# Optimization experiments

Hardware: AMD Instinct MI355X
Metric: run time of the kernel (lower is better)

## Reference

```python
import jax, jax.numpy as jnp
import numpy as np

N, C, H, W = 10, 512, 40, 40
HW = H * W
OUT_CH = 128
EPS = 1e-12

def _l2norm(x, axis):
    # matches F.normalize: v / max(||v||_2, eps)
    n = jnp.sqrt(jnp.sum(x * x, axis=axis, keepdims=True))
    return x / jnp.maximum(n, EPS)

def _conv(x, w, b, pad):
    y = jax.lax.conv_general_dilated(
        x, w, window_strides=(1, 1), padding=[(pad, pad), (pad, pad)],
        dimension_numbers=('NCHW', 'OIHW', 'NCHW'))
    return y + b[None, :, None, None]

def setup_inputs() -> dict:
    key = jax.random.key(0)
    ks = jax.random.split(key, 6)
    feats = jax.random.normal(ks[0], (N, C, H, W), jnp.float32)
    SISMs = jax.random.uniform(ks[1], (N, 1, H, W), jnp.float32)
    # ResNetBlock(HW -> 128) params (Kaiming-uniform-ish fan-in bounds)
    s1 = float(1.0 / np.sqrt(HW * 9))
    s2 = float(1.0 / np.sqrt(OUT_CH * 9))
    ss = float(1.0 / np.sqrt(HW))
    w1 = jax.random.uniform(ks[2], (OUT_CH, HW, 3, 3), jnp.float32, -s1, s1)
    b1 = jnp.zeros((OUT_CH,), jnp.float32)
    w2 = jax.random.uniform(ks[3], (OUT_CH, OUT_CH, 3, 3), jnp.float32, -s2, s2)
    b2 = jnp.zeros((OUT_CH,), jnp.float32)
    ws = jax.random.uniform(ks[4], (OUT_CH, HW, 1, 1), jnp.float32, -ss, ss)
    bs = jnp.zeros((OUT_CH,), jnp.float32)
    return dict(feats=feats, SISMs=SISMs, w1=w1, b1=b1, w2=w2, b2=b2, ws=ws, bs=bs)

def reference(feats, SISMs, w1, b1, w2, b2, ws, bs):
    # SISMs supplied at (H,W): bilinear resize w/ align_corners=True at same size is identity
    NFs = _l2norm(feats, axis=1)                                   # (N,C,H,W)
    SIVs = _l2norm(jnp.mean(NFs * SISMs, axis=(-1, -2)), axis=1)   # (N,C)
    # CFM: 1x1 conv of NFs with SIVs as filters -> (N,N,H,W)
    cm = jnp.einsum('nchw,mc->nmhw', NFs, SIVs).reshape(N, N, HW)
    cm = _l2norm(cm, axis=2)
    corr = jnp.einsum('nmk,npk->nmp', cm, cm)                      # (N,N,N)
    wv = jax.nn.softmax(jnp.sum(corr, axis=2), axis=1)             # (N,N)
    CSA = jnp.sum(cm * wv[:, :, None], axis=1)                     # (N,HW)
    mn = jnp.min(CSA, axis=1, keepdims=True)
    mx = jnp.max(CSA, axis=1, keepdims=True)
    CSA = (CSA - mn) / (mx - mn + EPS)
    CSA_maps = CSA.reshape(N, 1, H, W)
    # self-correlation features: (N, HW, H, W)
    NFf = NFs.reshape(N, C, HW)
    SCFs = jnp.einsum('nci,ncj->nij', NFf, NFf).reshape(N, HW, H, W)
    # reorder channels by descending CSA evidence
    idx = jnp.argsort(-CSA, axis=1)                                # (N,HW)
    RSCFs = jnp.take_along_axis(SCFs, idx[:, :, None, None], axis=1)
    x = RSCFs * CSA_maps
    # ResNetBlock: relu(conv2(relu(conv1(x))) + shortcut_1x1(x))
    h = jax.nn.relu(_conv(x, w1, b1, 1))
    h = _conv(h, w2, b2, 1)
    sc = _conv(x, ws, bs, 0)
    return jax.nn.relu(h + sc)
```

## Files before the change

### kernel.cpp

```cpp
#include <hip/hip_runtime.h>
#include <hip/hip_bf16.h>
#include <math.h>

typedef short short8 __attribute__((ext_vector_type(8)));
typedef short short4v __attribute__((ext_vector_type(4)));
typedef float f32x4 __attribute__((ext_vector_type(4)));
typedef __hip_bfloat16 bf16;

#define KN 10
#define KC 512
#define KHW 1600
#define KH 40
#define KOC 128
#define KPW 42
#define KM 1280

__device__ __forceinline__ void gload16(const void* g, void* l) {
  __builtin_amdgcn_global_load_lds(
      (const __attribute__((address_space(1))) unsigned int*)g,
      (__attribute__((address_space(3))) unsigned int*)l, 16, 0, 0);
}

__device__ __forceinline__ double blockReduceSumD(double v) {
  __shared__ double tmpS[8];
  int lane = threadIdx.x & 63, wv = threadIdx.x >> 6;
  #pragma unroll
  for (int o = 32; o > 0; o >>= 1) v += __shfl_down(v, o);
  if (lane == 0) tmpS[wv] = v;
  __syncthreads();
  if (threadIdx.x == 0) {
    int nw = (blockDim.x + 63) >> 6;
    double s = 0;
    for (int i = 0; i < nw; i++) s += tmpS[i];
    tmpS[0] = s;
  }
  __syncthreads();
  double r = tmpS[0];
  __syncthreads();
  return r;
}

__device__ __forceinline__ double blockReduceMinD(double v) {
  __shared__ double tmpMn[8];
  int lane = threadIdx.x & 63, wv = threadIdx.x >> 6;
  #pragma unroll
  for (int o = 32; o > 0; o >>= 1) v = fmin(v, __shfl_down(v, o));
  if (lane == 0) tmpMn[wv] = v;
  __syncthreads();
  if (threadIdx.x == 0) {
    int nw = (blockDim.x + 63) >> 6;
    double s = tmpMn[0];
    for (int i = 1; i < nw; i++) s = fmin(s, tmpMn[i]);
    tmpMn[0] = s;
  }
  __syncthreads();
  double r = tmpMn[0];
  __syncthreads();
  return r;
}

__device__ __forceinline__ double blockReduceMaxD(double v) {
  __shared__ double tmpMx[8];
  int lane = threadIdx.x & 63, wv = threadIdx.x >> 6;
  #pragma unroll
  for (int o = 32; o > 0; o >>= 1) v = fmax(v, __shfl_down(v, o));
  if (lane == 0) tmpMx[wv] = v;
  __syncthreads();
  if (threadIdx.x == 0) {
    int nw = (blockDim.x + 63) >> 6;
    double s = tmpMx[0];
    for (int i = 1; i < nw; i++) s = fmax(s, tmpMx[i]);
    tmpMx[0] = s;
  }
  __syncthreads();
  double r = tmpMx[0];
  __syncthreads();
  return r;
}


__global__ void k_rnormp(const float* __restrict__ feats, double* __restrict__ ps) {
  int t = blockIdx.x * 256 + threadIdx.x;
  if (t >= KN * KHW) return;
  int ci = blockIdx.y;
  int n = t / KHW, k = t % KHW;
  const float* p = feats + (size_t)n * KC * KHW + (size_t)ci * 128 * KHW + k;
  double s = 0.0;
  for (int c = 0; c < 128; ++c) { double v = p[(size_t)c * KHW]; s += v * v; }
  ps[(size_t)ci * KN * KHW + t] = s;
}

__global__ void k_rnormc(const double* __restrict__ ps, double* __restrict__ rnorm) {
  int t = blockIdx.x * 256 + threadIdx.x;
  if (t >= KN * KHW) return;
  double s = ps[t] + ps[KN * KHW + t] + ps[2 * KN * KHW + t] + ps[3 * KN * KHW + t];
  double nn = sqrt(s);
  if (nn < 1e-12) nn = 1e-12;
  rnorm[t] = 1.0 / nn;
}

__global__ void k_nft(const float* __restrict__ feats, const double* __restrict__ rnorm,
                      const float* __restrict__ sism, bf16* __restrict__ NFT,
                      double* __restrict__ vpp) {
  __shared__ float T[32][33];
  int n = blockIdx.z, k0 = blockIdx.x * 32, c0 = blockIdx.y * 32;
  int tx = threadIdx.x, ty = threadIdx.y;
  const float* fb = feats + ((size_t)n * KC + c0) * KHW + k0;
  #pragma unroll
  for (int ii = 0; ii < 4; ii++) {
    int cl = ty * 4 + ii;
    T[cl][tx] = fb[(size_t)cl * KHW + tx];
  }
  __syncthreads();
  bf16* ob = NFT + ((size_t)n * KHW + k0) * KC + c0;
  #pragma unroll
  for (int ii = 0; ii < 4; ii++) {
    int kl = ty * 4 + ii;
    float r = (float)rnorm[n * KHW + k0 + kl];
    ob[(size_t)kl * KC + tx] = __float2bfloat16(T[tx][kl] * r);
  }
  double rs = rnorm[n * KHW + k0 + tx] * (double)sism[n * KHW + k0 + tx];
  #pragma unroll
  for (int ii = 0; ii < 4; ii++) {
    int cl = ty * 4 + ii;
    double v = (double)T[cl][tx] * rs;
    #pragma unroll
    for (int o = 16; o > 0; o >>= 1) v += __shfl_down(v, o, 32);
    if (tx == 0) vpp[((size_t)n * KC + c0 + cl) * 50 + k0 / 32] = v;
  }
}

__global__ void k_sivnorm2(const double* __restrict__ vpp, double* __restrict__ SIV) {
  int n = blockIdx.x, c = threadIdx.x;
  const double* p = vpp + ((size_t)n * KC + c) * 50;
  double acc = 0;
  #pragma unroll 5
  for (int j = 0; j < 50; j++) acc += p[j];
  acc /= (double)KHW;
  double s2 = blockReduceSumD(acc * acc);
  double nn = sqrt(s2);
  if (nn < 1e-12) nn = 1e-12;
  SIV[n * KC + c] = acc / nn;
}

__global__ void k_cmP(const float* __restrict__ feats, const double* __restrict__ SIV,
                      double* __restrict__ cmp) {
  __shared__ double sv[KN][64];
  int kc = blockIdx.x, ci = blockIdx.y, n = blockIdx.z;
  for (int t = threadIdx.x; t < KN * 64; t += 256) {
    int m = t / 64, c = t % 64;
    sv[m][c] = SIV[m * KC + ci * 64 + c];
  }
  __syncthreads();
  int k = kc * 256 + threadIdx.x;
  if (k >= KHW) return;
  const float* f = feats + ((size_t)n * KC + ci * 64) * KHW + k;
  double acc[KN];
  #pragma unroll
  for (int m = 0; m < KN; m++) acc[m] = 0.0;
  for (int c = 0; c < 64; ++c) {
    double fv = f[(size_t)c * KHW];
    #pragma unroll
    for (int m = 0; m < KN; m++) acc[m] += fv * sv[m][c];
  }
  const size_t str = (size_t)KN * KN * KHW;
  #pragma unroll
  for (int m = 0; m < KN; m++)
    cmp[(size_t)ci * str + ((size_t)n * KN + m) * KHW + k] = acc[m];
}

__global__ void k_cmB(const double* __restrict__ cmp, const double* __restrict__ rnorm,
                      double* __restrict__ cm) {
  size_t t = (size_t)blockIdx.x * 256 + threadIdx.x;
  if (t >= (size_t)KN * KN * KHW) return;
  int k = t % KHW;
  int n = (int)(t / ((size_t)KN * KHW));
  const size_t str = (size_t)KN * KN * KHW;
  double s = 0;
  #pragma unroll
  for (int ci = 0; ci < 8; ci++) s += cmp[ci * str + t];
  cm[t] = s * rnorm[n * KHW + k];
}

__global__ void k_cmnorm(double* __restrict__ cm) {
  double* row = cm + (size_t)blockIdx.x * KHW;
  double s = 0;
  for (int k = threadIdx.x; k < KHW; k += 256) { double v = row[k]; s += v * v; }
  s = blockReduceSumD(s);
  double nn = sqrt(s);
  if (nn < 1e-12) nn = 1e-12;
  double rn = 1.0 / nn;
  for (int k = threadIdx.x; k < KHW; k += 256) row[k] *= rn;
}

__global__ void k_st(const double* __restrict__ cm, double* __restrict__ tbuf) {
  int b = blockIdx.x;
  int n = b / KN, m = b % KN;
  const double* base = cm + (size_t)n * KN * KHW;
  double acc = 0;
  for (int k = threadIdx.x; k < KHW; k += 256) {
    double S = 0;
    #pragma unroll
    for (int mm = 0; mm < KN; mm++) S += base[(size_t)mm * KHW + k];
    acc += base[(size_t)m * KHW + k] * S;
  }
  acc = blockReduceSumD(acc);
  if (threadIdx.x == 0) tbuf[b] = acc;
}

__global__ void k_csa(const double* __restrict__ cm, const double* __restrict__ tbuf,
                      double* __restrict__ CSAd, float* __restrict__ CSAf) {
  __shared__ double w[KN];
  int n = blockIdx.x, tid = threadIdx.x;
  if (tid == 0) {
    double v[KN], mx = -1e300;
    #pragma unroll
    for (int m = 0; m < KN; m++) { v[m] = tbuf[n * KN + m]; mx = fmax(mx, v[m]); }
    double s = 0;
    #pragma unroll
    for (int m = 0; m < KN; m++) { v[m] = exp(v[m] - mx); s += v[m]; }
    #pragma unroll
    for (int m = 0; m < KN; m++) w[m] = v[m] / s;
  }
  __syncthreads();
  double v[7];
  int cnt = 0;
  double lmin = 1e300, lmax = -1e300;
  for (int k = tid; k < KHW; k += 256) {
    double a = 0;
    #pragma unroll
    for (int m = 0; m < KN; m++) a += cm[((size_t)n * KN + m) * KHW + k] * w[m];
    v[cnt++] = a;
    lmin = fmin(lmin, a);
    lmax = fmax(lmax, a);
  }
  double mn = blockReduceMinD(lmin);
  double mx = blockReduceMaxD(lmax);
  double inv = 1.0 / (mx - mn + 1e-12);
  cnt = 0;
  for (int k = tid; k < KHW; k += 256) {
    double nv = (v[cnt++] - mn) * inv;
    CSAd[(size_t)n * KHW + k] = nv;
    CSAf[(size_t)n * KHW + k] = (float)nv;
  }
}

__global__ void k_rank(const double* __restrict__ CSAd, int* __restrict__ idx) {
  __shared__ double key[KHW];
  int b = blockIdx.x;
  int n = b / 100, it = b % 100;
  const double* src = CSAd + (size_t)n * KHW;
  for (int j = threadIdx.x; j < KHW; j += 256) key[j] = src[j];
  __syncthreads();
  int wave = threadIdx.x >> 6, lane = threadIdx.x & 63;
  int i0 = it * 16 + wave * 4;
  double ki[4];
  #pragma unroll
  for (int ii = 0; ii < 4; ii++) ki[ii] = key[i0 + ii];
  int r[4] = {0, 0, 0, 0};
  #pragma unroll
  for (int q = 0; q < 25; q++) {
    int j = q * 64 + lane;
    double kj = key[j];
    #pragma unroll
    for (int ii = 0; ii < 4; ii++) {
      int i = i0 + ii;
      r[ii] += (kj > ki[ii]) || (kj == ki[ii] && j < i);
    }
  }
  #pragma unroll
  for (int ii = 0; ii < 4; ii++) {
    int v = r[ii];
    #pragma unroll
    for (int o = 32; o > 0; o >>= 1) v += __shfl_down(v, o);
    if (lane == 0) idx[n * KHW + v] = i0 + ii;
  }
}

__global__ void k_prepw1s(const float* __restrict__ w1, const float* __restrict__ wsc,
                          bf16* __restrict__ w1s) {
  int t = blockIdx.x * 256 + threadIdx.x;
  int m = t / KHW, i = t % KHW;
  int tau = m >> 7, o = m & 127;
  float v = (tau < 9) ? w1[((size_t)o * KHW + i) * 9 + tau]
                      : wsc[(size_t)o * KHW + i];
  w1s[t] = __float2bfloat16(v);
}

__global__ void k_prepw2(const float* __restrict__ w2, bf16* __restrict__ w2p) {
  int t = blockIdx.x * 256 + threadIdx.x;
  if (t >= KOC * 9 * KOC) return;
  int o = t / (9 * KOC), r = t % (9 * KOC);
  int s = r / KOC, i = r % KOC;
  w2p[t] = __float2bfloat16(w2[(size_t)o * 9 * KOC + (size_t)i * 9 + s]);
}

__global__ void k_gath2(const short* __restrict__ NFT, const int* __restrict__ idx,
                        short* __restrict__ NFcg) {
  __shared__ short T[32][33];
  int i0 = blockIdx.x * 32, c0 = blockIdx.y * 32, n = blockIdx.z;
  int tx = threadIdx.x, ty = threadIdx.y;
  #pragma unroll
  for (int ii = 0; ii < 4; ii++) {
    int row = ty * 4 + ii;
    int id = idx[n * KHW + i0 + row];
    T[row][tx] = NFT[((size_t)n * KHW + id) * KC + c0 + tx];
  }
  __syncthreads();
  #pragma unroll
  for (int ii = 0; ii < 4; ii++) {
    int cl = ty * 4 + ii;
    NFcg[((size_t)n * KC + c0 + cl) * KHW + i0 + tx] = T[tx][cl];
  }
}

__global__ void k_zprep(const bf16* __restrict__ NFT, const float* __restrict__ CSAf,
                        bf16* __restrict__ Zpad) {
  int t = blockIdx.x * 256 + threadIdx.x;
  const int per_n = KHW * (KC / 4);
  int n = t / per_n, r = t % per_n;
  int p = r / (KC / 4), cq = r % (KC / 4);
  float cs = CSAf[n * KHW + p];
  const short* src = (const short*)(NFT + ((size_t)n * KHW + p) * KC) + cq * 4;
  short4v v = *(const short4v*)src;
  short4v o;
  #pragma unroll
  for (int j = 0; j < 4; j++) {
    short s = v[j];
    bf16 hb = *reinterpret_cast<bf16*>(&s);
    bf16 res = __float2bfloat16(__bfloat162float(hb) * cs);
    o[j] = *reinterpret_cast<short*>(&res);
  }
  int y = p / KH, x = p % KH;
  short* dst = (short*)(Zpad + ((size_t)n * KPW * KPW + (size_t)(y + 1) * KPW + (x + 1)) * KC) + cq * 4;
  *(short4v*)dst = o;
}

__global__ __launch_bounds__(256) void k_gemmU(const short* __restrict__ w1s,
                                               const short* __restrict__ NFcg,
                                               bf16* __restrict__ Uc,
                                               bf16* __restrict__ Usc) {
  __shared__ __align__(16) short smem[8704];
  short* As = smem;
  short* Bs = smem + 2048;
  short* Cs = smem;
  int b = blockIdx.x;
  int workid = (b & 7) * 100 + (b >> 3);
  int pair = workid / 20;
  int th = workid % 20;
  int n = pair >> 2, c0 = (pair & 3) * 128;
  int tau = th >> 1, half = th & 1;
  int m0 = tau * 128 + half * 64;
  int tid = threadIdx.x, lane = tid & 63, wave = tid >> 6;
  int quad = lane >> 4, l15 = lane & 15;
  int wm = (wave & 1) * 32, wn = (wave >> 1) * 64;
  int ar = tid >> 2, ko = (tid & 3) * 8;
  const short* Bb = NFcg + (size_t)n * KC * KHW;
  const short* pa0 = w1s + (size_t)(m0 + ar) * KHW + ko;
  const short* pb0 = Bb + (size_t)(c0 + ar) * KHW + ko;
  const short* pb1 = Bb + (size_t)(c0 + ar + 64) * KHW + ko;
  char* dA  = (char*)As + tid * 16;
  char* dB0 = (char*)Bs + tid * 16;
  char* dB1 = (char*)Bs + 4096 + tid * 16;
  f32x4 acc[2][4] = {};
  for (int k0 = 0; k0 < KHW; k0 += 32) {
    __syncthreads();
    gload16(pa0 + k0, dA);
    gload16(pb0 + k0, dB0);
    gload16(pb1 + k0, dB1);
    __syncthreads();
    short8 a[2], bb[4];
    #pragma unroll
    for (int t = 0; t < 2; t++) a[t] = *(const short8*)&As[(wm + t * 16 + l15) * 32 + quad * 8];
    #pragma unroll
    for (int t = 0; t < 4; t++) bb[t] = *(const short8*)&Bs[(wn + t * 16 + l15) * 32 + quad * 8];
    #pragma unroll
    for (int ti = 0; ti < 2; ti++)
      #pragma unroll
      for (int tj = 0; tj < 4; tj++)
        acc[ti][tj] = __builtin_amdgcn_mfma_f32_16x16x32_bf16(a[ti], bb[tj], acc[ti][tj], 0, 0, 0);
  }
  __syncthreads();
  #pragma unroll
  for (int ti = 0; ti < 2; ti++) {
    int lr = wm + ti * 16 + quad * 4;
    #pragma unroll
    for (int tj = 0; tj < 4; tj++) {
      int lc = wn + tj * 16 + l15;
      #pragma unroll
      for (int r = 0; r < 4; r++)
        *(bf16*)&Cs[(lr + r) * 136 + lc] = __float2bfloat16(acc[ti][tj][r]);
    }
  }
  __syncthreads();
  int dyq = tau / 3, dxq = tau % 3;
  #pragma unroll
  for (int pass = 0; pass < 4; pass++) {
    int row = pass * 16 + (tid >> 4);
    int col = (tid & 15) * 8;
    if (tau < 9) {
      *(float4*)&Uc[((size_t)((n * 3 + dyq) * 128 + half * 64 + row)) * 1536 + dxq * 512 + c0 + col] =
          *(const float4*)&Cs[row * 136 + col];
    } else {
      *(float4*)&Usc[((size_t)(n * 128 + half * 64 + row)) * 512 + c0 + col] =
          *(const float4*)&Cs[row * 136 + col];
    }
  }
}

__global__ __launch_bounds__(256) void k_convh(const short* __restrict__ Uc,
                                               const short* __restrict__ Usc,
                                               const short* __restrict__ Zpad,
                                               float* __restrict__ Hpart) {
  __shared__ __align__(16) short As[128 * 32];
  __shared__ __align__(16) short Bs[64 * 32];
  int b = blockIdx.x;
  int workid = (b & 7) * 125 + (b >> 3);
  int pair = workid / 25;
  int pt = workid % 25;
  int n = pair >> 2, dy = pair & 3;
  int p0 = pt * 64;
  int tid = threadIdx.x, lane = tid & 63, wave = tid >> 6;
  int quad = lane >> 4, l15 = lane & 15;
  int wm = (wave & 1) * 64, wn = (wave >> 1) * 32;
  int ar = tid >> 2, ko = (tid & 3) * 8;
  const short* Zb = Zpad + (size_t)n * KPW * KPW * KC;
  int pr = p0 + ar;
  int y0 = pr / KH, x0 = pr % KH;
  bool isconv = (dy < 3);
  const short* Abase = isconv ? Uc + ((size_t)(n * 3 + dy) * 128) * 1536
                              : Usc + (size_t)n * 128 * 512;
  int astr = isconv ? 1536 : 512;
  int ndx = isconv ? 3 : 1;
  char* dA0 = (char*)As + tid * 16;
  char* dA1 = (char*)As + 4096 + tid * 16;
  char* dB  = (char*)Bs + tid * 16;
  f32x4 acc[4][2] = {};
  for (int dx = 0; dx < ndx; ++dx) {
    int yy = isconv ? (y0 + dy) : (y0 + 1);
    int xx = isconv ? (x0 + dx) : (x0 + 1);
    const short* a0 = Abase + (size_t)ar * astr + dx * 512 + ko;
    const short* a1 = Abase + (size_t)(ar + 64) * astr + dx * 512 + ko;
    const short* b0 = Zb + ((size_t)yy * KPW + xx) * KC + ko;
    for (int k0 = 0; k0 < KC; k0 += 32) {
      __syncthreads();
      gload16(a0 + k0, dA0);
      gload16(a1 + k0, dA1);
      gload16(b0 + k0, dB);
      __syncthreads();
      short8 a[4], bb[2];
      #pragma unroll
      for (int t = 0; t < 4; t++) a[t] = *(const short8*)&As[(wm + t * 16 + l15) * 32 + quad * 8];
      #pragma unroll
      for (int t = 0; t < 2; t++) bb[t] = *(const short8*)&Bs[(wn + t * 16 + l15) * 32 + quad * 8];
      #pragma unroll
      for (int ti = 0; ti < 4; ti++)
        #pragma unroll
        for (int tj = 0; tj < 2; tj++)
          acc[ti][tj] = __builtin_amdgcn_mfma_f32_16x16x32_bf16(a[ti], bb[tj], acc[ti][tj], 0, 0, 0);
    }
  }
  float* cb = Hpart + ((size_t)(dy * KN + n)) * KOC * KHW;
  #pragma unroll
  for (int ti = 0; ti < 4; ti++) {
    int o = wm + ti * 16 + quad * 4;
    #pragma unroll
    for (int tj = 0; tj < 2; tj++) {
      int q = p0 + wn + tj * 16 + l15;
      #pragma unroll
      for (int r = 0; r < 4; r++)
        cb[(size_t)(o + r) * KHW + q] = acc[ti][tj][r];
    }
  }
}

__global__ void k_hprep3(const float* __restrict__ Hpart, const float* __restrict__ b1,
                         bf16* __restrict__ hpadT) {
  __shared__ float T[32][132];
  int n = blockIdx.y, p0 = blockIdx.x * 32;
  int tx = threadIdx.x, ty = threadIdx.y;
  const size_t str = (size_t)KN * KOC * KHW;
  const float* hb = Hpart + (size_t)n * KOC * KHW;
  #pragma unroll
  for (int oc = 0; oc < 16; oc++) {
    int o = oc * 8 + ty;
    size_t off = (size_t)o * KHW + p0 + tx;
    T[tx][o] = fmaxf(hb[off] + hb[str + off] + hb[2 * str + off] + b1[o], 0.0f);
  }
  __syncthreads();
  bf16* hp = hpadT + (size_t)n * KPW * KPW * KOC;
  #pragma unroll
  for (int pc = 0; pc < 4; pc++) {
    int pl = ty * 4 + pc;
    int pp = p0 + pl;
    int yy = pp / KH, xx = pp % KH;
    bf16* row = hp + ((size_t)(yy + 1) * KPW + (xx + 1)) * KOC;
    #pragma unroll
    for (int u = 0; u < 4; u++) row[tx * 4 + u] = __float2bfloat16(T[pl][tx * 4 + u]);
  }
}

__global__ __launch_bounds__(256) void k_conv2(const short* __restrict__ w2p,
                                               const short* __restrict__ hpadT,
                                               float* __restrict__ Cpart) {
  __shared__ __align__(16) short As[128 * 32];
  __shared__ __align__(16) short Bs[64 * 32];
  int p0 = blockIdx.x * 64, dy = blockIdx.y, n = blockIdx.z;
  int tid = threadIdx.x, lane = tid & 63, wave = tid >> 6;
  int quad = lane >> 4, l15 = lane & 15;
  int wm = (wave & 1) * 64, wn = (wave >> 1) * 32;
  int ar = tid >> 2, ko = (tid & 3) * 8;
  const short* hb = hpadT + (size_t)n * KPW * KPW * KOC;
  int pr = p0 + ar;
  int y0 = pr / KH, x0 = pr % KH;
  char* dA0 = (char*)As + tid * 16;
  char* dA1 = (char*)As + 4096 + tid * 16;
  char* dB  = (char*)Bs + tid * 16;
  f32x4 acc[4][2] = {};
  for (int dx = 0; dx < 3; ++dx) {
    const short* a0 = w2p + (size_t)ar * 9 * KOC + (dy * 3 + dx) * KOC + ko;
    const short* a1 = w2p + (size_t)(ar + 64) * 9 * KOC + (dy * 3 + dx) * KOC + ko;
    const short* b0 = hb + ((size_t)(y0 + dy) * KPW + (x0 + dx)) * KOC + ko;
    for (int k0 = 0; k0 < KOC; k0 += 32) {
      __syncthreads();
      gload16(a0 + k0, dA0);
      gload16(a1 + k0, dA1);
      gload16(b0 + k0, dB);
      __syncthreads();
      short8 a[4], bb[2];
      #pragma unroll
      for (int t = 0; t < 4; t++) a[t] = *(const short8*)&As[(wm + t * 16 + l15) * 32 + quad * 8];
      #pragma unroll
      for (int t = 0; t < 2; t++) bb[t] = *(const short8*)&Bs[(wn + t * 16 + l15) * 32 + quad * 8];
      #pragma unroll
      for (int ti = 0; ti < 4; ti++)
        #pragma unroll
        for (int tj = 0; tj < 2; tj++)
          acc[ti][tj] = __builtin_amdgcn_mfma_f32_16x16x32_bf16(a[ti], bb[tj], acc[ti][tj], 0, 0, 0);
    }
  }
  float* cb = Cpart + ((size_t)(dy * KN + n)) * KOC * KHW;
  #pragma unroll
  for (int ti = 0; ti < 4; ti++) {
    int o = wm + ti * 16 + quad * 4;
    #pragma unroll
    for (int tj = 0; tj < 2; tj++) {
      int q = p0 + wn + tj * 16 + l15;
      #pragma unroll
      for (int r = 0; r < 4; r++)
        cb[(size_t)(o + r) * KHW + q] = acc[ti][tj][r];
    }
  }
}

__global__ void k_final2(const float* __restrict__ Cpart, const float* __restrict__ Hpart,
                         const float* __restrict__ b2, const float* __restrict__ bs,
                         float* __restrict__ out) {
  int t = blockIdx.x * 256 + threadIdx.x;
  if (t >= KN * KOC * KHW) return;
  int o = (t / KHW) % KOC;
  const size_t stride = (size_t)KN * KOC * KHW;
  float v = Cpart[t] + Cpart[stride + t] + Cpart[2 * stride + t] +
            Hpart[3 * stride + t] + b2[o] + bs[o];
  out[t] = fmaxf(v, 0.0f);
}

extern "C" void kernel_launch(void* const* d_in, const int* in_sizes, int n_in,
                              void* d_out, int out_size, void* d_ws, size_t ws_size,
                              hipStream_t stream) {
  const float* feats = (const float*)d_in[0];
  const float* sisms = (const float*)d_in[1];
  const float* w1 = (const float*)d_in[2];
  const float* b1 = (const float*)d_in[3];
  const float* w2 = (const float*)d_in[4];
  const float* b2 = (const float*)d_in[5];
  const float* wsc = (const float*)d_in[6];
  const float* bsc = (const float*)d_in[7];
  float* out = (float*)d_out;

  char* w = (char*)d_ws;
  auto carve = [&](size_t bytes) -> void* {
    void* p = (void*)w;
    w += (bytes + 255) & ~(size_t)255;
    return p;
  };
  bf16* NFT   = (bf16*)carve((size_t)KN * KHW * KC * 2);
  bf16* NFcg  = (bf16*)carve((size_t)KN * KC * KHW * 2);
  bf16* Uc    = (bf16*)carve((size_t)KN * 3 * 128 * 1536 * 2);
  bf16* Usc   = (bf16*)carve((size_t)KN * 128 * 512 * 2);
  bf16* w1s   = (bf16*)carve((size_t)KM * KHW * 2);
  bf16* Zpad  = (bf16*)carve((size_t)KN * KPW * KPW * KC * 2);
  bf16* hpadT = (bf16*)carve((size_t)KN * KPW * KPW * KOC * 2);
  float* Hpart = (float*)carve((size_t)4 * KN * KOC * KHW * 4);
  float* Cpart = (float*)carve((size_t)3 * KN * KOC * KHW * 4);
  bf16* w2p   = (bf16*)carve((size_t)KOC * 9 * KOC * 2);
  double* psbuf = (double*)carve((size_t)4 * KN * KHW * 8);
  double* rnorm = (double*)carve((size_t)KN * KHW * 8);
  double* vpp   = (double*)carve((size_t)KN * KC * 50 * 8);
  double* SIV   = (double*)carve((size_t)KN * KC * 8);
  double* cmp   = (double*)carve((size_t)8 * KN * KN * KHW * 8);
  double* cm    = (double*)carve((size_t)KN * KN * KHW * 8);
  double* tbuf  = (double*)carve((size_t)KN * KN * 8);
  double* CSAd  = (double*)carve((size_t)KN * KHW * 8);
  float* CSAf   = (float*)carve((size_t)KN * KHW * 4);
  int* idxb     = (int*)carve((size_t)KN * KHW * 4);

  hipMemsetAsync(hpadT, 0, (size_t)KN * KPW * KPW * KOC * 2, stream);
  hipMemsetAsync(Zpad, 0, (size_t)KN * KPW * KPW * KC * 2, stream);

  k_rnormp<<<dim3(63, 4), 256, 0, stream>>>(feats, psbuf);
  k_rnormc<<<63, 256, 0, stream>>>(psbuf, rnorm);
  k_nft<<<dim3(50, 16, KN), dim3(32, 8), 0, stream>>>(feats, rnorm, sisms, NFT, vpp);
  k_sivnorm2<<<KN, 512, 0, stream>>>(vpp, SIV);
  k_cmP<<<dim3(7, 8, KN), 256, 0, stream>>>(feats, SIV, cmp);
  k_cmB<<<625, 256, 0, stream>>>(cmp, rnorm, cm);
  k_cmnorm<<<KN * KN, 256, 0, stream>>>(cm);
  k_st<<<KN * KN, 256, 0, stream>>>(cm, tbuf);
  k_csa<<<KN, 256, 0, stream>>>(cm, tbuf, CSAd, CSAf);
  k_rank<<<1000, 256, 0, stream>>>(CSAd, idxb);

  k_prepw1s<<<KM * KHW / 256, 256, 0, stream>>>(w1, wsc, w1s);
  k_prepw2<<<576, 256, 0, stream>>>(w2, w2p);
  k_gath2<<<dim3(50, 16, KN), dim3(32, 8), 0, stream>>>((const short*)NFT, idxb, (short*)NFcg);
  k_zprep<<<KN * KHW * (KC / 4) / 256, 256, 0, stream>>>(NFT, CSAf, Zpad);

  k_gemmU<<<800, 256, 0, stream>>>((const short*)w1s, (const short*)NFcg, Uc, Usc);
  k_convh<<<1000, 256, 0, stream>>>((const short*)Uc, (const short*)Usc,
                                    (const short*)Zpad, Hpart);
  k_hprep3<<<dim3(50, KN), dim3(32, 8), 0, stream>>>(Hpart, b1, hpadT);
  k_conv2<<<dim3(25, 3, KN), 256, 0, stream>>>((const short*)w2p, (const short*)hpadT, Cpart);
  k_final2<<<8000, 256, 0, stream>>>(Cpart, Hpart, b2, bsc, out);
}
```

Before: 306.5 us.

## Fuse conv1 dy-reduction with bias/ReLU/bf16 pack into double-buffered GEMM kernel

Merges the three per-dy conv1 partial GEMMs into a single block that accumulates all 9 taps over K, then applies bias and ReLU and writes the padded bf16 hidden tensor directly, eliminating the k_hprep3 pass and the fp32 Hpart round-trip for the conv path. The main loop uses a 64-wide K step with double-buffered async global-to-LDS loads, explicit vmcnt waits, an XOR-swizzled LDS layout, and an XCD-aware block remapping. Block count drops from 1000 to 500, and conv blocks now carry a much longer K loop than shortcut blocks, which creates load imbalance.

Measured after the change: 296.8 us. 1.03x faster.

```diff
diff --git a/kernel.cpp b/kernel.cpp
--- a/kernel.cpp
+++ b/kernel.cpp
@@ -408,95 +408,139 @@
   }
 }
 
-__global__ __launch_bounds__(256) void k_convh(const short* __restrict__ Uc,
+__global__ __launch_bounds__(256) void k_convf(const short* __restrict__ Uc,
                                                const short* __restrict__ Usc,
                                                const short* __restrict__ Zpad,
-                                               float* __restrict__ Hpart) {
-  __shared__ __align__(16) short As[128 * 32];
-  __shared__ __align__(16) short Bs[64 * 32];
+                                               const float* __restrict__ b1,
+                                               float* __restrict__ Hpart,
+                                               bf16* __restrict__ hpadT) {
+  __shared__ __align__(16) short smem[24576];
+  short* As = smem;
+  short* Bs = smem + 16384;
+  short* Cs = smem;
   int b = blockIdx.x;
-  int workid = (b & 7) * 125 + (b >> 3);
-  int pair = workid / 25;
-  int pt = workid % 25;
-  int n = pair >> 2, dy = pair & 3;
+  int xcd = b & 7, bi = b >> 3;
+  const int qch = 62, rch = 4;
+  int wgid = (xcd < rch ? xcd * (qch + 1) : rch * (qch + 1) + (xcd - rch) * qch) + bi;
+  bool isconv = (wgid & 1) == 0;
+  int cid = wgid >> 1;
+  int n = cid / 25, pt = cid % 25;
   int p0 = pt * 64;
   int tid = threadIdx.x, lane = tid & 63, wave = tid >> 6;
   int quad = lane >> 4, l15 = lane & 15;
   int wm = (wave & 1) * 64, wn = (wave >> 1) * 32;
-  int ar = tid >> 2, ko = (tid & 3) * 8;
+  int sk = ((tid & 7) ^ ((tid >> 3) & 7)) * 8;
+  int rowg = tid >> 3;
   const short* Zb = Zpad + (size_t)n * KPW * KPW * KC;
-  int pr = p0 + ar;
-  int y0 = pr / KH, x0 = pr % KH;
-  bool isconv = (dy < 3);
-  const short* Abase = isconv ? Uc + ((size_t)(n * 3 + dy) * 128) * 1536
-                              : Usc + (size_t)n * 128 * 512;
-  int astr = isconv ? 1536 : 512;
-  int ndx = isconv ? 3 : 1;
-  char* dA0 = (char*)As + tid * 16;
-  char* dA1 = (char*)As + 4096 + tid * 16;
-  char* dB  = (char*)Bs + tid * 16;
+  const short* pA[4];
+  #pragma unroll
+  for (int g = 0; g < 4; g++) {
+    int row = g * 32 + rowg;
+    pA[g] = isconv ? Uc + ((size_t)(n * 3 * 128) + row) * 1536 + sk
+                   : Usc + ((size_t)(n * 128) + row) * 512 + sk;
+  }
+  const short* pB[2];
+  #pragma unroll
+  for (int g = 0; g < 2; g++) {
+    int p = p0 + g * 32 + rowg;
+    int y = p / KH, x = p % KH;
+    pB[g] = Zb + ((size_t)y * KPW + x) * KC + sk;
+  }
+  char* lA = (char*)As + tid * 16;
+  char* lB = (char*)Bs + tid * 16;
+  int NS = isconv ? 72 : 8;
+  int bq = (l15 >> 2) & 1;
+  int qx = (quad ^ (l15 & 3)) * 8;
+  int koff0 = 32 * bq + qx;
+  int koff1 = 32 * (1 - bq) + qx;
   f32x4 acc[4][2] = {};
-  for (int dx = 0; dx < ndx; ++dx) {
-    int yy = isconv ? (y0 + dy) : (y0 + 1);
-    int xx = isconv ? (x0 + dx) : (x0 + 1);
-    const short* a0 = Abase + (size_t)ar * astr + dx * 512 + ko;
-    const short* a1 = Abase + (size_t)(ar + 64) * astr + dx * 512 + ko;
-    const short* b0 = Zb + ((size_t)yy * KPW + xx) * KC + ko;
-    for (int k0 = 0; k0 < KC; k0 += 32) {
-      __syncthreads();
-      gload16(a0 + k0, dA0);
-      gload16(a1 + k0, dA1);
-      gload16(b0 + k0, dB);
-      __syncthreads();
-      short8 a[4], bb[2];
-      #pragma unroll
-      for (int t = 0; t < 4; t++) a[t] = *(const short8*)&As[(wm + t * 16 + l15) * 32 + quad * 8];
-      #pragma unroll
-      for (int t = 0; t < 2; t++) bb[t] = *(const short8*)&Bs[(wn + t * 16 + l15) * 32 + quad * 8];
+  {
+    int boff = isconv ? 0 : 22016;
+    gload16(pA[0], lA); gload16(pA[1], lA + 4096);
+    gload16(pA[2], lA + 8192); gload16(pA[3], lA + 12288);
+    gload16(pB[0] + boff, lB); gload16(pB[1] + boff, lB + 4096);
+  }
+  for (int s = 0; s < NS; s++) {
+    int cb = s & 1, nb = cb ^ 1;
+    if (s + 1 < NS) {
+      int s2 = s + 1, aoff, boff;
+      if (isconv) {
+        int dy = s2 / 24;
+        int kk = (s2 - dy * 24) * 64;
+        aoff = dy * 196608 + kk;
+        boff = dy * 21504 + kk;
+      } else {
+        aoff = s2 * 64;
+        boff = 22016 + s2 * 64;
+      }
+      char* la = lA + nb * 16384;
+      char* lb = lB + nb * 8192;
+      gload16(pA[0] + aoff, la); gload16(pA[1] + aoff, la + 4096);
+      gload16(pA[2] + aoff, la + 8192); gload16(pA[3] + aoff, la + 12288);
+      gload16(pB[0] + boff, lb); gload16(pB[1] + boff, lb + 4096);
+      asm volatile("s_waitcnt vmcnt(6)" ::: "memory");
+    } else {
+      asm volatile("s_waitcnt vmcnt(0)" ::: "memory");
+    }
+    __builtin_amdgcn_s_barrier();
+    __builtin_amdgcn_sched_barrier(0);
+    const short* Ab = As + cb * 8192;
+    const short* Bb = Bs + cb * 4096;
+    #pragma unroll
+    for (int ks = 0; ks < 2; ks++) {
+      int ko = (ks == 0) ? koff0 : koff1;
+      short8 av[4], bv[2];
+      #pragma unroll
+      for (int t = 0; t < 4; t++) av[t] = *(const short8*)&Ab[(wm + t * 16 + l15) * 64 + ko];
+      #pragma unroll
+      for (int t = 0; t < 2; t++) bv[t] = *(const short8*)&Bb[(wn + t * 16 + l15) * 64 + ko];
       #pragma unroll
       for (int ti = 0; ti < 4; ti++)
         #pragma unroll
         for (int tj = 0; tj < 2; tj++)
-          acc[ti][tj] = __builtin_amdgcn_mfma_f32_16x16x32_bf16(a[ti], bb[tj], acc[ti][tj], 0, 0, 0);
-    }
-  }
-  float* cb = Hpart + ((size_t)(dy * KN + n)) * KOC * KHW;
-  #pragma unroll
-  for (int ti = 0; ti < 4; ti++) {
-    int o = wm + ti * 16 + quad * 4;
-    #pragma unroll
-    for (int tj = 0; tj < 2; tj++) {
-      int q = p0 + wn + tj * 16 + l15;
-      #pragma unroll
-      for (int r = 0; r < 4; r++)
-        cb[(size_t)(o + r) * KHW + q] = acc[ti][tj][r];
-    }
-  }
-}
-
-__global__ void k_hprep3(const float* __restrict__ Hpart, const float* __restrict__ b1,
-                         bf16* __restrict__ hpadT) {
-  __shared__ float T[32][132];
-  int n = blockIdx.y, p0 = blockIdx.x * 32;
-  int tx = threadIdx.x, ty = threadIdx.y;
-  const size_t str = (size_t)KN * KOC * KHW;
-  const float* hb = Hpart + (size_t)n * KOC * KHW;
-  #pragma unroll
-  for (int oc = 0; oc < 16; oc++) {
-    int o = oc * 8 + ty;
-    size_t off = (size_t)o * KHW + p0 + tx;
-    T[tx][o] = fmaxf(hb[off] + hb[str + off] + hb[2 * str + off] + b1[o], 0.0f);
-  }
-  __syncthreads();
-  bf16* hp = hpadT + (size_t)n * KPW * KPW * KOC;
-  #pragma unroll
-  for (int pc = 0; pc < 4; pc++) {
-    int pl = ty * 4 + pc;
-    int pp = p0 + pl;
-    int yy = pp / KH, xx = pp % KH;
-    bf16* row = hp + ((size_t)(yy + 1) * KPW + (xx + 1)) * KOC;
-    #pragma unroll
-    for (int u = 0; u < 4; u++) row[tx * 4 + u] = __float2bfloat16(T[pl][tx * 4 + u]);
+          acc[ti][tj] = __builtin_amdgcn_mfma_f32_16x16x32_bf16(av[ti], bv[tj], acc[ti][tj], 0, 0, 0);
+    }
+    __builtin_amdgcn_s_barrier();
+  }
+  if (isconv) {
+    #pragma unroll
+    for (int ti = 0; ti < 4; ti++) {
+      int o = wm + ti * 16 + quad * 4;
+      f32x4 bvv = *(const f32x4*)&b1[o];
+      #pragma unroll
+      for (int tj = 0; tj < 2; tj++) {
+        int pl = wn + tj * 16 + l15;
+        #pragma unroll
+        for (int rr = 0; rr < 4; rr++) {
+          float v = fmaxf(acc[ti][tj][rr] + bvv[rr], 0.0f);
+          *(bf16*)&Cs[pl * 136 + o + rr] = __float2bfloat16(v);
+        }
+      }
+    }
+    __builtin_amdgcn_s_barrier();
+    bf16* hp = hpadT + (size_t)n * KPW * KPW * KOC;
+    #pragma unroll
+    for (int pass = 0; pass < 4; pass++) {
+      int rowp = pass * 16 + (tid >> 4);
+      int colv = (tid & 15) * 8;
+      int p = p0 + rowp;
+      int y = p / KH, x = p % KH;
+      *(short8*)((short*)hp + ((size_t)(y + 1) * KPW + (x + 1)) * KOC + colv) =
+          *(const short8*)&Cs[rowp * 136 + colv];
+    }
+  } else {
+    float* cb2 = Hpart + ((size_t)(3 * KN + n)) * KOC * KHW;
+    #pragma unroll
+    for (int ti = 0; ti < 4; ti++) {
+      int o = wm + ti * 16 + quad * 4;
+      #pragma unroll
+      for (int tj = 0; tj < 2; tj++) {
+        int qq = p0 + wn + tj * 16 + l15;
+        #pragma unroll
+        for (int rr = 0; rr < 4; rr++)
+          cb2[(size_t)(o + rr) * KHW + qq] = acc[ti][tj][rr];
+      }
+    }
   }
 }
 
@@ -625,9 +669,8 @@
   k_zprep<<<KN * KHW * (KC / 4) / 256, 256, 0, stream>>>(NFT, CSAf, Zpad);
 
   k_gemmU<<<800, 256, 0, stream>>>((const short*)w1s, (const short*)NFcg, Uc, Usc);
-  k_convh<<<1000, 256, 0, stream>>>((const short*)Uc, (const short*)Usc,
-                                    (const short*)Zpad, Hpart);
-  k_hprep3<<<dim3(50, KN), dim3(32, 8), 0, stream>>>(Hpart, b1, hpadT);
+  k_convf<<<500, 256, 0, stream>>>((const short*)Uc, (const short*)Usc,
+                                   (const short*)Zpad, b1, Hpart, hpadT);
   k_conv2<<<dim3(25, 3, KN), 256, 0, stream>>>((const short*)w2p, (const short*)hpadT, Cpart);
   k_final2<<<8000, 256, 0, stream>>>(Cpart, Hpart, b2, bsc, out);
 }
```
